# Optimization experiments

Hardware: AMD Instinct MI355X
Metric: run time of the kernel (lower is better)

The kernel has to match this reference:

```python
import jax, jax.numpy as jnp
import numpy as np

B, T, H = 16, 512, 384   # batch, phoneme length, hidden
F, K = 384, 3            # filter size, kernel size
DMAX = 8                 # max per-token duration
L = T * DMAX             # static max expanded length (original uses real_len.max())


def conv1d_same(x, w, b):
    # x: [B, T, Cin], w: [Cout, Cin, K] (torch OIW layout), padding = K//2 both sides
    y = jax.lax.conv_general_dilated(
        x.transpose(0, 2, 1), w, window_strides=(1,),
        padding=[(K // 2, K // 2)], dimension_numbers=('NCW', 'OIW', 'NCW'))
    return y.transpose(0, 2, 1) + b


def layer_norm(x, g, b, eps=1e-5):
    mu = jnp.mean(x, axis=-1, keepdims=True)
    var = jnp.mean(jnp.square(x - mu), axis=-1, keepdims=True)
    return (x - mu) * jax.lax.rsqrt(var + eps) * g + b


def setup_inputs() -> dict:
    key = jax.random.key(0)
    ks = jax.random.split(key, 10)
    x = jax.random.normal(ks[0], (B, T, H), dtype=jnp.float32)
    # log-durations whose exp().round() gives integers in [1, DMAX]
    dur = jax.random.randint(ks[1], (B, T), 1, DMAX + 1)
    true_durations = jnp.log(dur.astype(jnp.float32))
    s1 = 1.0 / np.sqrt(H * K)
    s2 = 1.0 / np.sqrt(F * K)
    s3 = 1.0 / np.sqrt(F)
    return {
        'x': x,
        'true_durations': true_durations,
        'conv1_w': jax.random.uniform(ks[2], (F, H, K), jnp.float32, -s1, s1),
        'conv1_b': jnp.zeros((F,), jnp.float32),
        'ln1_g': jnp.ones((F,), jnp.float32),
        'ln1_b': jnp.zeros((F,), jnp.float32),
        'conv2_w': jax.random.uniform(ks[3], (F, F, K), jnp.float32, -s2, s2),
        'conv2_b': jnp.zeros((F,), jnp.float32),
        'ln2_g': jnp.ones((F,), jnp.float32),
        'ln2_b': jnp.zeros((F,), jnp.float32),
        'lin_w': jax.random.uniform(ks[4], (F, 1), jnp.float32, -s3, s3),
        'lin_b': jnp.zeros((1,), jnp.float32),
    }


def reference(x, true_durations, conv1_w, conv1_b, ln1_g, ln1_b,
              conv2_w, conv2_b, ln2_g, ln2_b, lin_w, lin_b):
    # duration predictor net (dropout in eval mode = identity)
    h = conv1d_same(x, conv1_w, conv1_b)
    h = jax.nn.gelu(layer_norm(h, ln1_g, ln1_b), approximate=False)
    h = conv1d_same(h, conv2_w, conv2_b)
    h = jax.nn.gelu(layer_norm(h, ln2_g, ln2_b), approximate=False)
    length = jax.nn.relu(h @ lin_w + lin_b)[..., 0]  # [B, T]

    # length regulation with ground-truth durations (detached ints in original)
    dur = jnp.round(jnp.exp(true_durations)).astype(jnp.int32)  # [B, T]
    ends = jnp.cumsum(dur, axis=1)          # [B, T]
    starts = ends - dur                     # [B, T]
    k = jnp.arange(L)                       # [L]
    # binary alignment: A[b,t,l] = 1 iff starts[b,t] <= l < ends[b,t]
    A = ((k >= starts[..., None]) & (k < ends[..., None])).astype(x.dtype)  # [B,T,L]
    out = jnp.einsum('bth,btl->blh', x, A)  # = (x^T @ A)^T, [B, L, H]
    return out, length
```

## Files before the change

kernel.cpp:

```cpp
#include <hip/hip_runtime.h>
#include <stdint.h>

typedef unsigned short u16;
typedef unsigned int   u32;

#define B_    16
#define T_    512
#define H_    384
#define F_    384
#define DMAX_ 8
#define L_    4096
#define KD    1152
#define M_    8192

typedef __bf16 bf16x8 __attribute__((ext_vector_type(8)));
typedef float  f32x4  __attribute__((ext_vector_type(4)));

typedef __attribute__((address_space(1))) u32 gu32;
typedef __attribute__((address_space(3))) u32 lu32;

__device__ __forceinline__ void dma16(const void* g, void* l) {
    __builtin_amdgcn_global_load_lds((gu32*)(uintptr_t)g, (lu32*)(u32)(uintptr_t)l, 16, 0, 0);
}

__device__ __forceinline__ u16 f2b(float f) {
    union { float f; u32 i; } v; v.f = f;
    u32 x = v.i;
    return (u16)((x + 0x7fffu + ((x >> 16) & 1u)) >> 16);
}
__device__ __forceinline__ float b2f(u16 u) {
    union { u32 i; float f; } v; v.i = ((u32)u) << 16; return v.f;
}

__global__ void k_durmap(const float* __restrict__ td, int* __restrict__ tmap) {
    __shared__ int s[T_];
    int b = blockIdx.x, t = threadIdx.x;
    int d = (int)roundf(expf(td[b * T_ + t]));
    if (d < 0) d = 0; if (d > DMAX_) d = DMAX_;
    int v = d;
    s[t] = v;
    __syncthreads();
    for (int off = 1; off < T_; off <<= 1) {
        int add = (t >= off) ? s[t - off] : 0;
        __syncthreads();
        v += add;
        s[t] = v;
        __syncthreads();
    }
    int end = v, start = end - d;
    for (int i = start; i < end; ++i) tmap[b * L_ + i] = t;
    int total = s[T_ - 1];
    for (int l = total + t; l < L_; l += T_) tmap[b * L_ + l] = -1;
}

__global__ void k_expand(const float* __restrict__ x, const int* __restrict__ tmap,
                         float* __restrict__ out) {
    int v = blockIdx.x * blockDim.x + threadIdx.x;
    if (v >= B_ * L_ * 96) return;
    int row = v / 96, c4 = v % 96;
    int b = row >> 12;
    int t = tmap[row];
    uint4 val = make_uint4(0u, 0u, 0u, 0u);
    if (t >= 0) val = *(const uint4*)(x + (size_t)((b << 9) + t) * H_ + c4 * 4);
    *(uint4*)(out + (size_t)row * H_ + c4 * 4) = val;
}

__global__ void k_xcast(const float* __restrict__ x, u16* __restrict__ xb) {
    int v = blockIdx.x * blockDim.x + threadIdx.x;
    if (v >= M_ * 96) return;
    float4 f = *(const float4*)(x + (size_t)v * 4);
    u16 o[4] = { f2b(f.x), f2b(f.y), f2b(f.z), f2b(f.w) };
    *(uint2*)(xb + (size_t)v * 4) = *(uint2*)o;
}

__global__ void k_repack(const float* __restrict__ w1, const float* __restrict__ w2,
                         u16* __restrict__ Wp1, u16* __restrict__ Wp2,
                         u16* __restrict__ zp) {
    int i = blockIdx.x * blockDim.x + threadIdx.x;
    if (i < 512) zp[i] = 0;
    const int n = F_ * H_ * 3;
    if (i >= 2 * n) return;
    const float* src = (i < n) ? w1 : w2;
    u16* dst         = (i < n) ? Wp1 : Wp2;
    int j = (i < n) ? i : i - n;
    int f = j / (H_ * 3);
    int rem = j % (H_ * 3);
    int c = rem / 3, kk = rem % 3;
    dst[f * KD + kk * H_ + c] = f2b(src[j]);
}

__launch_bounds__(256, 3)
__global__ void k_gemm(const u16* __restrict__ src, const u16* __restrict__ Wp,
                       const float* __restrict__ bias, u16* __restrict__ Hb,
                       const u16* __restrict__ zp) {
    __shared__ u16 smem[1280 * 8];
    int tid = threadIdx.x;
    int w = tid >> 6, lane = tid & 63;
    int quad = lane >> 4, l16 = lane & 15;
    int m0 = blockIdx.x * 32;
    int n0 = blockIdx.y * 128;

    int rowA = tid >> 3;
    int qlA  = (tid & 7) ^ (rowA & 7);
    int coffA = qlA * 8;
    int arow = m0 + rowA;
    int bB = arow >> 9, tt = arow & 511;
    const u16* abase[3];
    #pragma unroll
    for (int kk = 0; kk < 3; ++kk) {
        int ts = tt + kk - 1;
        abase[kk] = (ts >= 0 && ts < T_) ? (src + (size_t)((bB << 9) + ts) * H_ + coffA)
                                         : (zp + coffA);
    }
    u16* destA = smem + (size_t)w * 512;
    const u16* bsrc[4];
    u16* destB[4];
    #pragma unroll
    for (int p = 0; p < 4; ++p) {
        int bc = tid + p * 256;
        int rowB = bc >> 3;
        int qlB  = (bc & 7) ^ (rowB & 7);
        bsrc[p]  = Wp + (size_t)(n0 + rowB) * KD + qlB * 8;
        destB[p] = smem + (size_t)((p + 1) * 256 + w * 64) * 8;
    }

    const u16* aptr[2][2];
    const u16* bptr[2][2];
    #pragma unroll
    for (int i = 0; i < 2; ++i)
        #pragma unroll
        for (int kv = 0; kv < 2; ++kv) {
            int row = i * 16 + l16;
            aptr[i][kv] = smem + (size_t)((row << 3) | ((kv * 4 + quad) ^ (row & 7))) * 8;
        }
    #pragma unroll
    for (int j = 0; j < 2; ++j)
        #pragma unroll
        for (int kv = 0; kv < 2; ++kv) {
            int row = w * 32 + j * 16 + l16;
            bptr[j][kv] = smem + (size_t)(256 + ((row << 3) | ((kv * 4 + quad) ^ (row & 7)))) * 8;
        }

    f32x4 acc[2][2];
    #pragma unroll
    for (int i = 0; i < 2; ++i)
        #pragma unroll
        for (int j = 0; j < 2; ++j)
            acc[i][j] = f32x4{0.f, 0.f, 0.f, 0.f};

    #pragma unroll
    for (int kk = 0; kk < 3; ++kk) {
        #pragma unroll
        for (int s = 0; s < 6; ++s) {
            int k0 = kk * 384 + s * 64;
            dma16(abase[kk] + s * 64, destA);
            #pragma unroll
            for (int p = 0; p < 4; ++p) dma16(bsrc[p] + k0, destB[p]);
            __syncthreads();

            bf16x8 af[2][2], bf[2][2];
            #pragma unroll
            for (int i = 0; i < 2; ++i)
                #pragma unroll
                for (int kv = 0; kv < 2; ++kv) af[i][kv] = *(const bf16x8*)aptr[i][kv];
            #pragma unroll
            for (int j = 0; j < 2; ++j)
                #pragma unroll
                for (int kv = 0; kv < 2; ++kv) bf[j][kv] = *(const bf16x8*)bptr[j][kv];
            #pragma unroll
            for (int kv = 0; kv < 2; ++kv)
                #pragma unroll
                for (int i = 0; i < 2; ++i)
                    #pragma unroll
                    for (int j = 0; j < 2; ++j)
                        acc[i][j] = __builtin_amdgcn_mfma_f32_16x16x32_bf16(af[i][kv], bf[j][kv], acc[i][j], 0, 0, 0);
            __syncthreads();
        }
    }

    #pragma unroll
    for (int i = 0; i < 2; ++i) {
        #pragma unroll
        for (int j = 0; j < 2; ++j) {
            int row = m0 + i * 16 + quad * 4;
            int col = n0 + w * 32 + j * 16 + l16;
            float bb = bias[col];
            #pragma unroll
            for (int r = 0; r < 4; ++r)
                Hb[(size_t)(row + r) * F_ + col] = f2b(acc[i][j][r] + bb);
        }
    }
}

__global__ void k_lngelu(const u16* __restrict__ Hin, const float* __restrict__ g,
                         const float* __restrict__ bta, u16* __restrict__ G) {
    int row = blockIdx.x;
    int lane = threadIdx.x;
    const u16* hr = Hin + (size_t)row * F_;
    float vals[6];
    float s = 0.f, s2 = 0.f;
    #pragma unroll
    for (int j = 0; j < 6; ++j) {
        float xv = b2f(hr[lane + j * 64]);
        vals[j] = xv; s += xv; s2 += xv * xv;
    }
    #pragma unroll
    for (int off = 32; off; off >>= 1) { s += __shfl_down(s, off); s2 += __shfl_down(s2, off); }
    s = __shfl(s, 0); s2 = __shfl(s2, 0);
    float mean = s * (1.f / F_);
    float var  = s2 * (1.f / F_) - mean * mean;
    float rstd = rsqrtf(var + 1e-5f);
    #pragma unroll
    for (int j = 0; j < 6; ++j) {
        int c = lane + j * 64;
        float y  = (vals[j] - mean) * rstd * g[c] + bta[c];
        float gl = 0.5f * y * (1.f + erff(y * 0.70710678118654752f));
        G[(size_t)row * F_ + c] = f2b(gl);
    }
}

__global__ void k_len(const u16* __restrict__ Hin, const float* __restrict__ g,
                      const float* __restrict__ bta, const float* __restrict__ lw,
                      const float* __restrict__ lb, float* __restrict__ lenout) {
    int row = blockIdx.x;
    int lane = threadIdx.x;
    const u16* hr = Hin + (size_t)row * F_;
    float vals[6];
    float s = 0.f, s2 = 0.f;
    #pragma unroll
    for (int j = 0; j < 6; ++j) {
        float xv = b2f(hr[lane + j * 64]);
        vals[j] = xv; s += xv; s2 += xv * xv;
    }
    #pragma unroll
    for (int off = 32; off; off >>= 1) { s += __shfl_down(s, off); s2 += __shfl_down(s2, off); }
    s = __shfl(s, 0); s2 = __shfl(s2, 0);
    float mean = s * (1.f / F_);
    float var  = s2 * (1.f / F_) - mean * mean;
    float rstd = rsqrtf(var + 1e-5f);
    float dot = 0.f;
    #pragma unroll
    for (int j = 0; j < 6; ++j) {
        int c = lane + j * 64;
        float y  = (vals[j] - mean) * rstd * g[c] + bta[c];
        float gl = 0.5f * y * (1.f + erff(y * 0.70710678118654752f));
        dot += gl * lw[c];
    }
    #pragma unroll
    for (int off = 32; off; off >>= 1) dot += __shfl_down(dot, off);
    if (lane == 0) {
        float r = dot + lb[0];
        lenout[row] = fmaxf(r, 0.f);
    }
}

extern "C" void kernel_launch(void* const* d_in, const int* in_sizes, int n_in,
                              void* d_out, int out_size, void* d_ws, size_t ws_size,
                              hipStream_t stream) {
    const float* x   = (const float*)d_in[0];
    const float* td  = (const float*)d_in[1];
    const float* w1  = (const float*)d_in[2];
    const float* b1  = (const float*)d_in[3];
    const float* g1  = (const float*)d_in[4];
    const float* be1 = (const float*)d_in[5];
    const float* w2  = (const float*)d_in[6];
    const float* b2  = (const float*)d_in[7];
    const float* g2  = (const float*)d_in[8];
    const float* be2 = (const float*)d_in[9];
    const float* lw  = (const float*)d_in[10];
    const float* lb  = (const float*)d_in[11];

    float* out0 = (float*)d_out;
    float* out1 = out0 + (size_t)B_ * L_ * H_;

    char* ws = (char*)d_ws;
    size_t off = 0;
    auto carve = [&](size_t bytes) -> void* {
        void* p = ws + off;
        off = (off + bytes + 255) & ~(size_t)255;
        return p;
    };
    int*  tmap = (int*)carve((size_t)B_ * L_ * sizeof(int));
    u16*  Wp1  = (u16*)carve((size_t)F_ * KD * sizeof(u16));
    u16*  Wp2  = (u16*)carve((size_t)F_ * KD * sizeof(u16));
    u16*  xb   = (u16*)carve((size_t)M_ * H_ * sizeof(u16));
    u16*  G    = (u16*)carve((size_t)M_ * F_ * sizeof(u16));
    u16*  zp   = (u16*)carve(1024);
    u16*  Hb   = (u16*)carve((size_t)M_ * F_ * sizeof(u16));

    k_durmap<<<B_, T_, 0, stream>>>(td, tmap);
    k_expand<<<(B_ * L_ * 96 + 255) / 256, 256, 0, stream>>>(x, tmap, out0);

    k_repack<<<(2 * F_ * H_ * 3 + 255) / 256, 256, 0, stream>>>(w1, w2, Wp1, Wp2, zp);
    k_xcast<<<(M_ * 96 + 255) / 256, 256, 0, stream>>>(x, xb);
    k_gemm<<<dim3(M_ / 32, 3), 256, 0, stream>>>(xb, Wp1, b1, Hb, zp);
    k_lngelu<<<M_, 64, 0, stream>>>(Hb, g1, be1, G);
    k_gemm<<<dim3(M_ / 32, 3), 256, 0, stream>>>(G, Wp2, b2, Hb, zp);
    k_len<<<M_, 64, 0, stream>>>(Hb, g2, be2, lw, lb, out1);
}
```

Baseline: 197.9 us.

## Fuse LayerNorm+GELU into full-width conv GEMMs and merge prep kernels

Each conv GEMM block now computes all 384 output columns for its 32 rows, so LayerNorm, GELU and, for the second conv, the final linear+ReLU run in the GEMM epilogue using cross-wave shared-memory reductions. This removes the bf16 intermediate H buffer and the two separate row-wise kernels. The duration map, weight repack and x cast are merged into one launch. The trade-off is a 3x smaller grid (256 blocks), more accumulator registers and about 53KB of LDS per block, which may reduce occupancy and the number of blocks per CU.

```diff
diff --git a/kernel.cpp b/kernel.cpp
--- a/kernel.cpp
+++ b/kernel.cpp
@@ -28,29 +28,50 @@
     u32 x = v.i;
     return (u16)((x + 0x7fffu + ((x >> 16) & 1u)) >> 16);
 }
-__device__ __forceinline__ float b2f(u16 u) {
-    union { u32 i; float f; } v; v.i = ((u32)u) << 16; return v.f;
-}
-
-__global__ void k_durmap(const float* __restrict__ td, int* __restrict__ tmap) {
-    __shared__ int s[T_];
-    int b = blockIdx.x, t = threadIdx.x;
-    int d = (int)roundf(expf(td[b * T_ + t]));
-    if (d < 0) d = 0; if (d > DMAX_) d = DMAX_;
-    int v = d;
-    s[t] = v;
-    __syncthreads();
-    for (int off = 1; off < T_; off <<= 1) {
-        int add = (t >= off) ? s[t - off] : 0;
-        __syncthreads();
-        v += add;
+
+__global__ void k_prep(const float* __restrict__ td, const float* __restrict__ w1,
+                       const float* __restrict__ w2, const float* __restrict__ x,
+                       int* __restrict__ tmap, u16* __restrict__ Wp1,
+                       u16* __restrict__ Wp2, u16* __restrict__ xb,
+                       u16* __restrict__ zp) {
+    int blk = blockIdx.x, tid = threadIdx.x;
+    if (blk < 16) {
+        __shared__ int s[T_];
+        int b = blk, t = tid;
+        int d = (int)roundf(expf(td[b * T_ + t]));
+        if (d < 0) d = 0; if (d > DMAX_) d = DMAX_;
+        int v = d;
         s[t] = v;
         __syncthreads();
-    }
-    int end = v, start = end - d;
-    for (int i = start; i < end; ++i) tmap[b * L_ + i] = t;
-    int total = s[T_ - 1];
-    for (int l = total + t; l < L_; l += T_) tmap[b * L_ + l] = -1;
+        for (int off = 1; off < T_; off <<= 1) {
+            int add = (t >= off) ? s[t - off] : 0;
+            __syncthreads();
+            v += add;
+            s[t] = v;
+            __syncthreads();
+        }
+        int end = v, start = end - d;
+        for (int i = start; i < end; ++i) tmap[b * L_ + i] = t;
+        int total = s[T_ - 1];
+        for (int l = total + t; l < L_; l += T_) tmap[b * L_ + l] = -1;
+    } else if (blk == 16) {
+        zp[tid] = 0;
+    } else if (blk < 17 + 1728) {
+        int j = (blk - 17) * 512 + tid;
+        const int n = F_ * H_ * 3;
+        const float* src = (j < n) ? w1 : w2;
+        u16* dst         = (j < n) ? Wp1 : Wp2;
+        int jj = (j < n) ? j : j - n;
+        int f = jj / (H_ * 3);
+        int rem = jj % (H_ * 3);
+        int c = rem / 3, kk = rem % 3;
+        dst[f * KD + kk * H_ + c] = f2b(src[jj]);
+    } else {
+        int v = (blk - 1745) * 512 + tid;
+        float4 f = *(const float4*)(x + (size_t)v * 4);
+        u16 o[4] = { f2b(f.x), f2b(f.y), f2b(f.z), f2b(f.w) };
+        *(uint2*)(xb + (size_t)v * 4) = *(uint2*)o;
+    }
 }
 
 __global__ void k_expand(const float* __restrict__ x, const int* __restrict__ tmap,
@@ -65,192 +86,219 @@
     *(uint4*)(out + (size_t)row * H_ + c4 * 4) = val;
 }
 
-__global__ void k_xcast(const float* __restrict__ x, u16* __restrict__ xb) {
-    int v = blockIdx.x * blockDim.x + threadIdx.x;
-    if (v >= M_ * 96) return;
-    float4 f = *(const float4*)(x + (size_t)v * 4);
-    u16 o[4] = { f2b(f.x), f2b(f.y), f2b(f.z), f2b(f.w) };
-    *(uint2*)(xb + (size_t)v * 4) = *(uint2*)o;
-}
-
-__global__ void k_repack(const float* __restrict__ w1, const float* __restrict__ w2,
-                         u16* __restrict__ Wp1, u16* __restrict__ Wp2,
-                         u16* __restrict__ zp) {
-    int i = blockIdx.x * blockDim.x + threadIdx.x;
-    if (i < 512) zp[i] = 0;
-    const int n = F_ * H_ * 3;
-    if (i >= 2 * n) return;
-    const float* src = (i < n) ? w1 : w2;
-    u16* dst         = (i < n) ? Wp1 : Wp2;
-    int j = (i < n) ? i : i - n;
-    int f = j / (H_ * 3);
-    int rem = j % (H_ * 3);
-    int c = rem / 3, kk = rem % 3;
-    dst[f * KD + kk * H_ + c] = f2b(src[j]);
-}
-
-__launch_bounds__(256, 3)
-__global__ void k_gemm(const u16* __restrict__ src, const u16* __restrict__ Wp,
-                       const float* __restrict__ bias, u16* __restrict__ Hb,
-                       const u16* __restrict__ zp) {
-    __shared__ u16 smem[1280 * 8];
+struct GemmCtx {
+    const u16* abase[3];
+    const u16* bbase[12];
+    u16* destA;
+    u16* destB[12];
+    const u16* aptr[2][2];
+    const u16* bptr[6][2];
+};
+
+__device__ __forceinline__ void gemm_core(u16* smem, const u16* __restrict__ src,
+                                          const u16* __restrict__ Wp,
+                                          const u16* __restrict__ zp,
+                                          int m0, int tid, f32x4 acc[2][6]) {
+    int w = tid >> 6, lane = tid & 63;
+    int quad = lane >> 4, l16 = lane & 15;
+
+    int rowA = tid >> 3;
+    int qlA  = (tid & 7) ^ (rowA & 7);
+    int arow = m0 + rowA;
+    int bB = arow >> 9, tt = arow & 511;
+    const u16* abase[3];
+    #pragma unroll
+    for (int kk = 0; kk < 3; ++kk) {
+        int ts = tt + kk - 1;
+        abase[kk] = (ts >= 0 && ts < T_) ? (src + (size_t)((bB << 9) + ts) * H_ + qlA * 8)
+                                         : (zp + qlA * 8);
+    }
+    u16* destA = smem + (size_t)(w * 64) * 8;
+
+    const u16* bbase[12];
+    u16* destB[12];
+    #pragma unroll
+    for (int p = 0; p < 12; ++p) {
+        int bc = p * 256 + tid;
+        int rowB = bc >> 3;
+        int qlB = (bc & 7) ^ (rowB & 7);
+        bbase[p] = Wp + (size_t)rowB * KD + qlB * 8;
+        destB[p] = smem + (size_t)(256 + p * 256 + w * 64) * 8;
+    }
+
+    const u16* aptr[2][2];
+    #pragma unroll
+    for (int i = 0; i < 2; ++i)
+        #pragma unroll
+        for (int kv = 0; kv < 2; ++kv) {
+            int row = i * 16 + l16;
+            aptr[i][kv] = smem + (size_t)((row << 3) | ((kv * 4 + quad) ^ (row & 7))) * 8;
+        }
+    const u16* bptr[6][2];
+    #pragma unroll
+    for (int j = 0; j < 6; ++j)
+        #pragma unroll
+        for (int kv = 0; kv < 2; ++kv) {
+            int row = w * 96 + j * 16 + l16;
+            bptr[j][kv] = smem + (size_t)(256 + ((row << 3) | ((kv * 4 + quad) ^ (row & 7)))) * 8;
+        }
+
+    #pragma unroll
+    for (int i = 0; i < 2; ++i)
+        #pragma unroll
+        for (int j = 0; j < 6; ++j)
+            acc[i][j] = f32x4{0.f, 0.f, 0.f, 0.f};
+
+    for (int kk = 0; kk < 3; ++kk) {
+        for (int s6 = 0; s6 < 6; ++s6) {
+            int koff = kk * 384 + s6 * 64;
+            dma16(abase[kk] + s6 * 64, destA);
+            #pragma unroll
+            for (int p = 0; p < 12; ++p) dma16(bbase[p] + koff, destB[p]);
+            __syncthreads();
+            #pragma unroll
+            for (int kv = 0; kv < 2; ++kv) {
+                bf16x8 af0 = *(const bf16x8*)aptr[0][kv];
+                bf16x8 af1 = *(const bf16x8*)aptr[1][kv];
+                #pragma unroll
+                for (int j = 0; j < 6; ++j) {
+                    bf16x8 bf = *(const bf16x8*)bptr[j][kv];
+                    acc[0][j] = __builtin_amdgcn_mfma_f32_16x16x32_bf16(af0, bf, acc[0][j], 0, 0, 0);
+                    acc[1][j] = __builtin_amdgcn_mfma_f32_16x16x32_bf16(af1, bf, acc[1][j], 0, 0, 0);
+                }
+            }
+            __syncthreads();
+        }
+    }
+}
+
+__launch_bounds__(256)
+__global__ void k_gemm1(const u16* __restrict__ xb, const u16* __restrict__ Wp,
+                        const float* __restrict__ bias, const float* __restrict__ g,
+                        const float* __restrict__ beta, u16* __restrict__ G,
+                        const u16* __restrict__ zp) {
+    __shared__ u16 smem[3328 * 8];
     int tid = threadIdx.x;
     int w = tid >> 6, lane = tid & 63;
     int quad = lane >> 4, l16 = lane & 15;
     int m0 = blockIdx.x * 32;
-    int n0 = blockIdx.y * 128;
-
-    int rowA = tid >> 3;
-    int qlA  = (tid & 7) ^ (rowA & 7);
-    int coffA = qlA * 8;
-    int arow = m0 + rowA;
-    int bB = arow >> 9, tt = arow & 511;
-    const u16* abase[3];
-    #pragma unroll
-    for (int kk = 0; kk < 3; ++kk) {
-        int ts = tt + kk - 1;
-        abase[kk] = (ts >= 0 && ts < T_) ? (src + (size_t)((bB << 9) + ts) * H_ + coffA)
-                                         : (zp + coffA);
-    }
-    u16* destA = smem + (size_t)w * 512;
-    const u16* bsrc[4];
-    u16* destB[4];
-    #pragma unroll
-    for (int p = 0; p < 4; ++p) {
-        int bc = tid + p * 256;
-        int rowB = bc >> 3;
-        int qlB  = (bc & 7) ^ (rowB & 7);
-        bsrc[p]  = Wp + (size_t)(n0 + rowB) * KD + qlB * 8;
-        destB[p] = smem + (size_t)((p + 1) * 256 + w * 64) * 8;
-    }
-
-    const u16* aptr[2][2];
-    const u16* bptr[2][2];
-    #pragma unroll
-    for (int i = 0; i < 2; ++i)
-        #pragma unroll
-        for (int kv = 0; kv < 2; ++kv) {
-            int row = i * 16 + l16;
-            aptr[i][kv] = smem + (size_t)((row << 3) | ((kv * 4 + quad) ^ (row & 7))) * 8;
-        }
-    #pragma unroll
-    for (int j = 0; j < 2; ++j)
-        #pragma unroll
-        for (int kv = 0; kv < 2; ++kv) {
-            int row = w * 32 + j * 16 + l16;
-            bptr[j][kv] = smem + (size_t)(256 + ((row << 3) | ((kv * 4 + quad) ^ (row & 7)))) * 8;
-        }
-
-    f32x4 acc[2][2];
-    #pragma unroll
-    for (int i = 0; i < 2; ++i)
-        #pragma unroll
-        for (int j = 0; j < 2; ++j)
-            acc[i][j] = f32x4{0.f, 0.f, 0.f, 0.f};
-
-    #pragma unroll
-    for (int kk = 0; kk < 3; ++kk) {
-        #pragma unroll
-        for (int s = 0; s < 6; ++s) {
-            int k0 = kk * 384 + s * 64;
-            dma16(abase[kk] + s * 64, destA);
-            #pragma unroll
-            for (int p = 0; p < 4; ++p) dma16(bsrc[p] + k0, destB[p]);
-            __syncthreads();
-
-            bf16x8 af[2][2], bf[2][2];
-            #pragma unroll
-            for (int i = 0; i < 2; ++i)
-                #pragma unroll
-                for (int kv = 0; kv < 2; ++kv) af[i][kv] = *(const bf16x8*)aptr[i][kv];
-            #pragma unroll
-            for (int j = 0; j < 2; ++j)
-                #pragma unroll
-                for (int kv = 0; kv < 2; ++kv) bf[j][kv] = *(const bf16x8*)bptr[j][kv];
-            #pragma unroll
-            for (int kv = 0; kv < 2; ++kv)
-                #pragma unroll
-                for (int i = 0; i < 2; ++i)
-                    #pragma unroll
-                    for (int j = 0; j < 2; ++j)
-                        acc[i][j] = __builtin_amdgcn_mfma_f32_16x16x32_bf16(af[i][kv], bf[j][kv], acc[i][j], 0, 0, 0);
-            __syncthreads();
-        }
-    }
-
-    #pragma unroll
-    for (int i = 0; i < 2; ++i) {
-        #pragma unroll
-        for (int j = 0; j < 2; ++j) {
-            int row = m0 + i * 16 + quad * 4;
-            int col = n0 + w * 32 + j * 16 + l16;
-            float bb = bias[col];
-            #pragma unroll
-            for (int r = 0; r < 4; ++r)
-                Hb[(size_t)(row + r) * F_ + col] = f2b(acc[i][j][r] + bb);
-        }
-    }
-}
-
-__global__ void k_lngelu(const u16* __restrict__ Hin, const float* __restrict__ g,
-                         const float* __restrict__ bta, u16* __restrict__ G) {
-    int row = blockIdx.x;
-    int lane = threadIdx.x;
-    const u16* hr = Hin + (size_t)row * F_;
-    float vals[6];
-    float s = 0.f, s2 = 0.f;
+
+    f32x4 acc[2][6];
+    gemm_core(smem, xb, Wp, zp, m0, tid, acc);
+
+    float bcol[6], gcol[6], becol[6];
     #pragma unroll
     for (int j = 0; j < 6; ++j) {
-        float xv = b2f(hr[lane + j * 64]);
-        vals[j] = xv; s += xv; s2 += xv * xv;
-    }
-    #pragma unroll
-    for (int off = 32; off; off >>= 1) { s += __shfl_down(s, off); s2 += __shfl_down(s2, off); }
-    s = __shfl(s, 0); s2 = __shfl(s2, 0);
-    float mean = s * (1.f / F_);
-    float var  = s2 * (1.f / F_) - mean * mean;
-    float rstd = rsqrtf(var + 1e-5f);
+        int col = w * 96 + j * 16 + l16;
+        bcol[j] = bias[col]; gcol[j] = g[col]; becol[j] = beta[col];
+    }
+    float* sb  = (float*)smem;
+    float* s2b = (float*)smem + 128;
+    #pragma unroll
+    for (int i = 0; i < 2; ++i)
+        #pragma unroll
+        for (int r = 0; r < 4; ++r) {
+            float s = 0.f, s2 = 0.f;
+            #pragma unroll
+            for (int j = 0; j < 6; ++j) {
+                float y = acc[i][j][r] + bcol[j];
+                s += y; s2 += y * y;
+            }
+            #pragma unroll
+            for (int off = 8; off; off >>= 1) { s += __shfl_down(s, off); s2 += __shfl_down(s2, off); }
+            if (l16 == 0) {
+                int rl = i * 16 + quad * 4 + r;
+                sb[w * 32 + rl] = s; s2b[w * 32 + rl] = s2;
+            }
+        }
+    __syncthreads();
+    #pragma unroll
+    for (int i = 0; i < 2; ++i)
+        #pragma unroll
+        for (int r = 0; r < 4; ++r) {
+            int rl = i * 16 + quad * 4 + r;
+            float S  = sb[rl] + sb[32 + rl] + sb[64 + rl] + sb[96 + rl];
+            float S2 = s2b[rl] + s2b[32 + rl] + s2b[64 + rl] + s2b[96 + rl];
+            float mean = S * (1.f / F_);
+            float var  = S2 * (1.f / F_) - mean * mean;
+            float rstd = rsqrtf(var + 1e-5f);
+            #pragma unroll
+            for (int j = 0; j < 6; ++j) {
+                int col = w * 96 + j * 16 + l16;
+                float y  = (acc[i][j][r] + bcol[j] - mean) * rstd * gcol[j] + becol[j];
+                float gl = 0.5f * y * (1.f + erff(y * 0.70710678118654752f));
+                G[(size_t)(m0 + rl) * F_ + col] = f2b(gl);
+            }
+        }
+}
+
+__launch_bounds__(256)
+__global__ void k_gemm2(const u16* __restrict__ G, const u16* __restrict__ Wp,
+                        const float* __restrict__ bias, const float* __restrict__ g,
+                        const float* __restrict__ beta, const float* __restrict__ lw,
+                        const float* __restrict__ lb, float* __restrict__ out1,
+                        const u16* __restrict__ zp) {
+    __shared__ u16 smem[3328 * 8];
+    int tid = threadIdx.x;
+    int w = tid >> 6, lane = tid & 63;
+    int quad = lane >> 4, l16 = lane & 15;
+    int m0 = blockIdx.x * 32;
+
+    f32x4 acc[2][6];
+    gemm_core(smem, G, Wp, zp, m0, tid, acc);
+
+    float bcol[6], gcol[6], becol[6], lwcol[6];
     #pragma unroll
     for (int j = 0; j < 6; ++j) {
-        int c = lane + j * 64;
-        float y  = (vals[j] - mean) * rstd * g[c] + bta[c];
-        float gl = 0.5f * y * (1.f + erff(y * 0.70710678118654752f));
-        G[(size_t)row * F_ + c] = f2b(gl);
-    }
-}
-
-__global__ void k_len(const u16* __restrict__ Hin, const float* __restrict__ g,
-                      const float* __restrict__ bta, const float* __restrict__ lw,
-                      const float* __restrict__ lb, float* __restrict__ lenout) {
-    int row = blockIdx.x;
-    int lane = threadIdx.x;
-    const u16* hr = Hin + (size_t)row * F_;
-    float vals[6];
-    float s = 0.f, s2 = 0.f;
-    #pragma unroll
-    for (int j = 0; j < 6; ++j) {
-        float xv = b2f(hr[lane + j * 64]);
-        vals[j] = xv; s += xv; s2 += xv * xv;
-    }
-    #pragma unroll
-    for (int off = 32; off; off >>= 1) { s += __shfl_down(s, off); s2 += __shfl_down(s2, off); }
-    s = __shfl(s, 0); s2 = __shfl(s2, 0);
-    float mean = s * (1.f / F_);
-    float var  = s2 * (1.f / F_) - mean * mean;
-    float rstd = rsqrtf(var + 1e-5f);
-    float dot = 0.f;
-    #pragma unroll
-    for (int j = 0; j < 6; ++j) {
-        int c = lane + j * 64;
-        float y  = (vals[j] - mean) * rstd * g[c] + bta[c];
-        float gl = 0.5f * y * (1.f + erff(y * 0.70710678118654752f));
-        dot += gl * lw[c];
-    }
-    #pragma unroll
-    for (int off = 32; off; off >>= 1) dot += __shfl_down(dot, off);
-    if (lane == 0) {
-        float r = dot + lb[0];
-        lenout[row] = fmaxf(r, 0.f);
+        int col = w * 96 + j * 16 + l16;
+        bcol[j] = bias[col]; gcol[j] = g[col]; becol[j] = beta[col]; lwcol[j] = lw[col];
+    }
+    float* sb  = (float*)smem;
+    float* s2b = (float*)smem + 128;
+    float* db  = (float*)smem + 256;
+    #pragma unroll
+    for (int i = 0; i < 2; ++i)
+        #pragma unroll
+        for (int r = 0; r < 4; ++r) {
+            float s = 0.f, s2 = 0.f;
+            #pragma unroll
+            for (int j = 0; j < 6; ++j) {
+                float y = acc[i][j][r] + bcol[j];
+                s += y; s2 += y * y;
+            }
+            #pragma unroll
+            for (int off = 8; off; off >>= 1) { s += __shfl_down(s, off); s2 += __shfl_down(s2, off); }
+            if (l16 == 0) {
+                int rl = i * 16 + quad * 4 + r;
+                sb[w * 32 + rl] = s; s2b[w * 32 + rl] = s2;
+            }
+        }
+    __syncthreads();
+    #pragma unroll
+    for (int i = 0; i < 2; ++i)
+        #pragma unroll
+        for (int r = 0; r < 4; ++r) {
+            int rl = i * 16 + quad * 4 + r;
+            float S  = sb[rl] + sb[32 + rl] + sb[64 + rl] + sb[96 + rl];
+            float S2 = s2b[rl] + s2b[32 + rl] + s2b[64 + rl] + s2b[96 + rl];
+            float mean = S * (1.f / F_);
+            float var  = S2 * (1.f / F_) - mean * mean;
+            float rstd = rsqrtf(var + 1e-5f);
+            float dot = 0.f;
+            #pragma unroll
+            for (int j = 0; j < 6; ++j) {
+                float y  = (acc[i][j][r] + bcol[j] - mean) * rstd * gcol[j] + becol[j];
+                float gl = 0.5f * y * (1.f + erff(y * 0.70710678118654752f));
+                dot += gl * lwcol[j];
+            }
+            #pragma unroll
+            for (int off = 8; off; off >>= 1) dot += __shfl_down(dot, off);
+            if (l16 == 0) db[w * 32 + rl] = dot;
+        }
+    __syncthreads();
+    if (tid < 32) {
+        float d = db[tid] + db[32 + tid] + db[64 + tid] + db[96 + tid] + lb[0];
+        out1[m0 + tid] = fmaxf(d, 0.f);
     }
 }
 
@@ -286,15 +334,9 @@
     u16*  xb   = (u16*)carve((size_t)M_ * H_ * sizeof(u16));
     u16*  G    = (u16*)carve((size_t)M_ * F_ * sizeof(u16));
     u16*  zp   = (u16*)carve(1024);
-    u16*  Hb   = (u16*)carve((size_t)M_ * F_ * sizeof(u16));
-
-    k_durmap<<<B_, T_, 0, stream>>>(td, tmap);
+
+    k_prep<<<3281, 512, 0, stream>>>(td, w1, w2, x, tmap, Wp1, Wp2, xb, zp);
     k_expand<<<(B_ * L_ * 96 + 255) / 256, 256, 0, stream>>>(x, tmap, out0);
-
-    k_repack<<<(2 * F_ * H_ * 3 + 255) / 256, 256, 0, stream>>>(w1, w2, Wp1, Wp2, zp);
-    k_xcast<<<(M_ * 96 + 255) / 256, 256, 0, stream>>>(x, xb);
-    k_gemm<<<dim3(M_ / 32, 3), 256, 0, stream>>>(xb, Wp1, b1, Hb, zp);
-    k_lngelu<<<M_, 64, 0, stream>>>(Hb, g1, be1, G);
-    k_gemm<<<dim3(M_ / 32, 3), 256, 0, stream>>>(G, Wp2, b2, Hb, zp);
-    k_len<<<M_, 64, 0, stream>>>(Hb, g2, be2, lw, lb, out1);
-}
+    k_gemm1<<<M_ / 32, 256, 0, stream>>>(xb, Wp1, b1, g1, be1, G, zp);
+    k_gemm2<<<M_ / 32, 256, 0, stream>>>(G, Wp2, b2, g2, be2, lw, lb, out1, zp);
+}
```

Measured after the change: 206.1 us. +4.2%, slower.
